# Kernel tuning notes

Measured on AMD Instinct MI355X. Metric: run time of the kernel, lower is better.

The kernel has to match this reference:

```python
import jax, jax.numpy as jnp
import numpy as np

N_HEAD = 8

def setup_inputs() -> dict:
    key = jax.random.key(0)
    ks = jax.random.split(key, 5)
    N, C, T, V = 64, 128, 64, 25
    x = jax.random.normal(ks[0], (N, C, T, V), dtype=jnp.float32)
    Wa = jax.random.normal(ks[1], (C, C), dtype=jnp.float32) * (1.0 / np.sqrt(C))
    ba = jax.random.normal(ks[2], (C,), dtype=jnp.float32) * 0.01
    Wp = jax.random.normal(ks[3], (C, C), dtype=jnp.float32) * (1.0 / np.sqrt(C))
    bp = jax.random.normal(ks[4], (C,), dtype=jnp.float32) * 0.01
    temp = jnp.ones((N_HEAD, 1), dtype=jnp.float32)
    denom_bias = jnp.zeros((N_HEAD, 1, 1), dtype=jnp.float32)
    return {"x": x, "Wa": Wa, "ba": ba, "Wp": Wp, "bp": bp, "temp": temp, "denom_bias": denom_bias}

def reference(x, Wa, ba, Wp, bp, temp, denom_bias):
    # x: (N, C, T, V); eval mode (dropout = identity); residual = identity (in==out, stride==1)
    N, C, T, V = x.shape
    H = N_HEAD
    hd = C // H
    res = x
    # 1x1 conv c_attn
    w = jnp.einsum('nctv,oc->notv', x, Wa) + ba[None, :, None, None]
    # (N,H,hd,T,V) -> (N,H,T,V,hd) -> (N,H,T*V,hd)
    w = w.reshape(N, H, hd, T, V).transpose(0, 1, 3, 4, 2).reshape(N, H, T * V, hd)
    w_sq = w * w
    denom = jnp.maximum(jnp.cumsum(w_sq, axis=2), 1e-12)
    w_normed = w_sq / denom + denom_bias  # denom_bias (H,1,1) broadcasts
    tmp = jnp.sum(w_normed, axis=-1) * temp  # (N,H,L) * (H,1)
    Pi = jax.nn.softmax(tmp, axis=2)  # (N,H,L)
    dots = jnp.cumsum(w_sq * Pi[..., None], axis=2) / (jnp.cumsum(Pi, axis=2) + 1e-8)[..., None]
    attn = 1.0 / (1.0 + dots)
    y = -(w * Pi[..., None]) * attn  # (N,H,L,hd)
    y = y.reshape(N, H, T, V, hd).transpose(0, 1, 4, 2, 3).reshape(N, C, T, V)
    y = jnp.einsum('nctv,oc->notv', y, Wp) + bp[None, :, None, None]
    y = y + res
    return jax.nn.relu(y)
```

## Files before the change

kernel.cpp:

```cpp
#include <hip/hip_runtime.h>
#include <hip/hip_bf16.h>

#define N_S     64
#define C_CH    128
#define L_SEQ   1600
#define H_HEADS 8
#define HD      16
#define SEGN    64
#define SEGL    25
#define PADW    136
#define PADT    70
#define NHD     13312
#define NHU     26624

typedef __attribute__((ext_vector_type(8))) short bf16x8;
typedef __attribute__((ext_vector_type(4))) float f32x4;

__device__ inline unsigned short f2bf(float f) {
  return __builtin_bit_cast(unsigned short, __float2bfloat16(f));
}
__device__ inline float bflo(unsigned int u) { return __builtin_bit_cast(float, u << 16); }
__device__ inline float bfhi(unsigned int u) { return __builtin_bit_cast(float, u & 0xffff0000u); }
__device__ inline unsigned int pk(float a, float b) {
  return (unsigned int)f2bf(a) | ((unsigned int)f2bf(b) << 16);
}

template <int CTRL>
__device__ inline float dppadd(float x) {
  int r = __builtin_amdgcn_update_dpp(0, __builtin_bit_cast(int, x), CTRL, 0xF, 0xF, true);
  return x + __builtin_bit_cast(float, r);
}


__global__ __launch_bounds__(256) void k_gemm1(const float* __restrict__ x,
                                               const float* __restrict__ Wa,
                                               const float* __restrict__ ba,
                                               unsigned short* __restrict__ w3u) {
  __shared__ unsigned short was[128 * PADW];
  __shared__ unsigned short xs[128 * PADT];
  const int n = blockIdx.y;
  const int l0 = blockIdx.x * 64;
  const int t = threadIdx.x;
  const float* xn = x + (size_t)n * (C_CH * L_SEQ);

#pragma unroll
  for (int it = 0; it < 16; ++it) {
    int pos = it * 256 + t;
    int o = pos >> 5;
    int c4 = (pos & 31) << 2;
    float4 v = *reinterpret_cast<const float4*>(Wa + o * C_CH + c4);
    ushort4 u;
    u.x = f2bf(v.x); u.y = f2bf(v.y); u.z = f2bf(v.z); u.w = f2bf(v.w);
    *reinterpret_cast<ushort4*>(&was[o * PADW + c4]) = u;
  }
#pragma unroll
  for (int it = 0; it < 8; ++it) {
    int pos = it * 256 + t;
    int c = pos >> 4;
    int l4 = (pos & 15) << 2;
    float4 v = *reinterpret_cast<const float4*>(xn + (size_t)c * L_SEQ + l0 + l4);
    ushort4 u;
    u.x = f2bf(v.x); u.y = f2bf(v.y); u.z = f2bf(v.z); u.w = f2bf(v.w);
    *reinterpret_cast<ushort4*>(&xs[c * PADT + l4]) = u;
  }
  __syncthreads();

  const int wv = t >> 6;
  const int lane = t & 63;
  const int r16 = lane & 15;
  const int kg = lane >> 4;
  f32x4 acc[8];
#pragma unroll
  for (int ot = 0; ot < 8; ++ot) acc[ot] = (f32x4){0.f, 0.f, 0.f, 0.f};

#pragma unroll
  for (int ks = 0; ks < 4; ++ks) {
    bf16x8 a;
#pragma unroll
    for (int j = 0; j < 8; ++j)
      a[j] = (short)xs[(ks * 32 + kg * 8 + j) * PADT + wv * 16 + r16];
#pragma unroll
    for (int ot = 0; ot < 8; ++ot) {
      bf16x8 b = *reinterpret_cast<const bf16x8*>(&was[(ot * 16 + r16) * PADW + ks * 32 + kg * 8]);
      acc[ot] = __builtin_amdgcn_mfma_f32_16x16x32_bf16(a, b, acc[ot], 0, 0, 0);
    }
  }
  const int lbase = l0 + wv * 16 + kg * 4;
  unsigned int idxA[4];
#pragma unroll
  for (int i = 0; i < 4; ++i) {
    unsigned int l = (unsigned int)(lbase + i);
    unsigned int sg = l / 25u;
    unsigned int j = l - sg * 25u;
    idxA[i] = (j >> 1) * 2048u + sg * 32u + ((unsigned int)r16 << 1) + (j & 1u);
  }
  unsigned short* w3n = w3u + (size_t)(n * H_HEADS) * NHU;
#pragma unroll
  for (int ot = 0; ot < 8; ++ot) {
    float bav = ba[ot * 16 + r16];
    unsigned short* p = w3n + (size_t)ot * NHU;
#pragma unroll
    for (int i = 0; i < 4; ++i)
      p[idxA[i]] = f2bf(acc[ot][i] + bav);
  }
}

__global__ __launch_bounds__(1024) void k_scan(const unsigned int* __restrict__ w3d,
                                               unsigned int* __restrict__ y3d,
                                               const float* __restrict__ temp,
                                               const float* __restrict__ dbias) {
  __shared__ float stot[SEGN][17];
  __shared__ float red[16];

  const int nh = blockIdx.x;
  const int h = nh & 7;
  const int t = threadIdx.x;
  const int d = t & 15;
  const int lane = t & 63;
  const int wv = t >> 6;
  const int seg = t >> 4;
  const float tscale = temp[h];
  const float db16 = 16.f * dbias[h];
  const float M = fmaxf((16.f + db16) * tscale, db16 * tscale);
  const float A = tscale * 1.44269504088896f;
  const float B = (db16 * tscale - M) * 1.44269504088896f;

  unsigned int vp[13];
  const unsigned int* srcd = w3d + (size_t)nh * NHD;
#pragma unroll
  for (int ii = 0; ii < 13; ++ii) vp[ii] = srcd[ii * 1024 + t];

  float tot = 0.f;
#pragma unroll
  for (int i = 0; i < SEGL; ++i) {
    float v = (i & 1) ? bfhi(vp[i >> 1]) : bflo(vp[i >> 1]);
    tot += v * v;
  }
  stot[seg][d] = tot;
  __syncthreads();
  {
    float val = stot[lane][wv];
#pragma unroll
    for (int sh = 1; sh < 64; sh <<= 1) {
      float nv = __shfl_up(val, sh);
      if (lane >= sh) val += nv;
    }
    stot[lane][wv] = val;
  }
  __syncthreads();
  const float off = stot[seg][d] - tot;

  unsigned int ep[13];
  float run = off;
  float sAcc = 0.f, wpAcc = 0.f;
  float eprev = 0.f;
#pragma unroll
  for (int i = 0; i < SEGL; ++i) {
    float v = (i & 1) ? bfhi(vp[i >> 1]) : bflo(vp[i >> 1]);
    float wsq = v * v;
    run += wsq;
    float c = __fdividef(wsq, fmaxf(run, 1e-12f));
    c = dppadd<0x128>(c);
    c = dppadd<0x124>(c);
    c = dppadd<0x122>(c);
    c = dppadd<0x121>(c);
    float e = exp2f(fmaf(c, A, B));
    sAcc += e;
    wpAcc = fmaf(wsq, e, wpAcc);
    if (i & 1) ep[i >> 1] = pk(eprev, e); else eprev = e;
  }
  ep[12] = pk(eprev, 0.f);
  {
    float s = sAcc;
#pragma unroll
    for (int mask = 32; mask; mask >>= 1) s += __shfl_xor(s, mask);
    if (lane == 0) red[wv] = s;
  }
  __syncthreads();
  float S16 = 0.f;
#pragma unroll
  for (int i2 = 0; i2 < 16; ++i2) S16 += red[i2];
  const float S = S16 * 0.0625f;
  const float ninvS = -1.0f / S;
  const float epsS = 1e-8f * S;

  stot[seg][d] = wpAcc;
  if (d == 0) stot[seg][16] = sAcc;
  __syncthreads();
  {
    float val = stot[lane][wv];
#pragma unroll
    for (int sh = 1; sh < 64; sh <<= 1) {
      float nv = __shfl_up(val, sh);
      if (lane >= sh) val += nv;
    }
    stot[lane][wv] = val;
    if (wv == 0) {
      float val2 = stot[lane][16];
#pragma unroll
      for (int sh = 1; sh < 64; sh <<= 1) {
        float nv = __shfl_up(val2, sh);
        if (lane >= sh) val2 += nv;
      }
      stot[lane][16] = val2;
    }
  }
  __syncthreads();
  const float wp_off = stot[seg][d] - wpAcc;
  const float pi_off = stot[seg][16] - sAcc;

  {
    float run_wp = wp_off, run_pi = pi_off;
    float ylo = 0.f;
#pragma unroll
    for (int i = 0; i < SEGL; ++i) {
      float v = (i & 1) ? bfhi(vp[i >> 1]) : bflo(vp[i >> 1]);
      float e = (i & 1) ? bfhi(ep[i >> 1]) : bflo(ep[i >> 1]);
      run_pi += e;
      run_wp = fmaf(v * v, e, run_wp);
      float dn = run_pi + epsS;
      float y = (v * e) * __fdividef(dn, dn + run_wp) * ninvS;
      if (i & 1) vp[i >> 1] = pk(ylo, y); else ylo = y;
    }
    vp[12] = pk(ylo, 0.f);
  }
  unsigned int* dstd = y3d + (size_t)nh * NHD;
#pragma unroll
  for (int ii = 0; ii < 13; ++ii) dstd[ii * 1024 + t] = vp[ii];
}

__global__ __launch_bounds__(256) void k_gemm2(const unsigned short* __restrict__ y3u,
                                               const float* __restrict__ Wp,
                                               const float* __restrict__ bp,
                                               const float* __restrict__ x,
                                               float* __restrict__ out) {
  __shared__ unsigned short wps[128 * PADW];
  __shared__ unsigned short ys[128 * PADT];
  const int n = blockIdx.y;
  const int l0 = blockIdx.x * 64;
  const int t = threadIdx.x;

#pragma unroll
  for (int it = 0; it < 16; ++it) {
    int pos = it * 256 + t;
    int o = pos >> 5;
    int c4 = (pos & 31) << 2;
    float4 v = *reinterpret_cast<const float4*>(Wp + o * C_CH + c4);
    ushort4 u;
    u.x = f2bf(v.x); u.y = f2bf(v.y); u.z = f2bf(v.z); u.w = f2bf(v.w);
    *reinterpret_cast<ushort4*>(&wps[o * PADW + c4]) = u;
  }
#pragma unroll
  for (int k = 0; k < 32; ++k) {
    int e = k * 256 + t;
    int lloc = e >> 7;
    int c = e & 127;
    unsigned int l = (unsigned int)(l0 + lloc);
    unsigned int sg = l / 25u;
    unsigned int j = l - sg * 25u;
    unsigned short v = y3u[(size_t)(n * H_HEADS + (c >> 4)) * NHU +
                           (j >> 1) * 2048u + sg * 32u + ((unsigned int)(c & 15) << 1) + (j & 1u)];
    ys[c * PADT + lloc] = v;
  }
  __syncthreads();

  const int wv = t >> 6;
  const int lane = t & 63;
  const int r16 = lane & 15;
  const int kg = lane >> 4;
  f32x4 acc[8];
#pragma unroll
  for (int ot = 0; ot < 8; ++ot) acc[ot] = (f32x4){0.f, 0.f, 0.f, 0.f};

#pragma unroll
  for (int ks = 0; ks < 4; ++ks) {
    bf16x8 b;
#pragma unroll
    for (int j = 0; j < 8; ++j)
      b[j] = (short)ys[(ks * 32 + kg * 8 + j) * PADT + wv * 16 + r16];
#pragma unroll
    for (int ot = 0; ot < 8; ++ot) {
      bf16x8 a = *reinterpret_cast<const bf16x8*>(&wps[(ot * 16 + r16) * PADW + ks * 32 + kg * 8]);
      acc[ot] = __builtin_amdgcn_mfma_f32_16x16x32_bf16(a, b, acc[ot], 0, 0, 0);
    }
  }
  const int gl = l0 + wv * 16 + r16;
#pragma unroll
  for (int ot = 0; ot < 8; ++ot) {
#pragma unroll
    for (int i = 0; i < 4; ++i) {
      int o = ot * 16 + kg * 4 + i;
      size_t idx = (size_t)n * (C_CH * L_SEQ) + (size_t)o * L_SEQ + gl;
      float r = acc[ot][i] + bp[o] + x[idx];
      out[idx] = fmaxf(r, 0.f);
    }
  }
}

extern "C" void kernel_launch(void* const* d_in, const int* in_sizes, int n_in,
                              void* d_out, int out_size, void* d_ws, size_t ws_size,
                              hipStream_t stream) {
  const float* x     = (const float*)d_in[0];
  const float* Wa    = (const float*)d_in[1];
  const float* ba    = (const float*)d_in[2];
  const float* Wp    = (const float*)d_in[3];
  const float* bp    = (const float*)d_in[4];
  const float* temp  = (const float*)d_in[5];
  const float* dbias = (const float*)d_in[6];
  float* out = (float*)d_out;

  unsigned short* w3u = (unsigned short*)d_ws;
  unsigned short* y3u = w3u + (size_t)N_S * H_HEADS * NHU;

  k_gemm1<<<dim3(L_SEQ / 64, N_S), 256, 0, stream>>>(x, Wa, ba, w3u);
  k_scan<<<N_S * H_HEADS, 1024, 0, stream>>>((const unsigned int*)w3u, (unsigned int*)y3u, temp, dbias);
  k_gemm2<<<dim3(L_SEQ / 64, N_S), 256, 0, stream>>>(y3u, Wp, bp, x, out);
}
```

Baseline: 83.65 us.

## Fuse first projection GEMM into per-head scan kernel via shared-memory slab

Merges the c_attn GEMM into the scan kernel: each (sample, head) block computes its 16 output channels over the full sequence in 256-column chunks and stores them in a shared-memory slab laid out for the scan. This removes the intermediate global write/read of the projected activations and one launch. The scan result is written in plain channel-major layout so the second GEMM can load it with vectorized 16-byte loads. In exchange, every head block re-reads and re-converts the whole input sample, roughly 8x redundant x traffic. The large shared footprint and serial chunk loop may also limit occupancy.

```diff
diff --git a/kernel.cpp b/kernel.cpp
--- a/kernel.cpp
+++ b/kernel.cpp
@@ -9,9 +9,9 @@
 #define SEGN    64
 #define SEGL    25
 #define PADW    136
-#define PADT    70
-#define NHD     13312
-#define NHU     26624
+#define PADX    270
+#define PADY    72
+#define SROW    839
 
 typedef __attribute__((ext_vector_type(8))) short bf16x8;
 typedef __attribute__((ext_vector_type(4))) float f32x4;
@@ -31,93 +31,77 @@
   return x + __builtin_bit_cast(float, r);
 }
 
-
-__global__ __launch_bounds__(256) void k_gemm1(const float* __restrict__ x,
-                                               const float* __restrict__ Wa,
-                                               const float* __restrict__ ba,
-                                               unsigned short* __restrict__ w3u) {
-  __shared__ unsigned short was[128 * PADW];
-  __shared__ unsigned short xs[128 * PADT];
-  const int n = blockIdx.y;
-  const int l0 = blockIdx.x * 64;
+__global__ __launch_bounds__(1024) void k_fused(const float* __restrict__ x,
+                                                const float* __restrict__ Wa,
+                                                const float* __restrict__ ba,
+                                                const float* __restrict__ temp,
+                                                const float* __restrict__ dbias,
+                                                unsigned short* __restrict__ y2) {
+  __shared__ unsigned short was[16 * PADW];
+  __shared__ unsigned short xs[128 * PADX];
+  __shared__ unsigned int slabd[16 * SROW];
+  __shared__ float stot[SEGN][17];
+  __shared__ float red[16];
+  unsigned short* slab = (unsigned short*)slabd;
+
+  const int bid = blockIdx.x;
+  const int nh = (bid & 7) * 64 + (bid >> 3);
+  const int n = nh >> 3;
+  const int h = nh & 7;
   const int t = threadIdx.x;
-  const float* xn = x + (size_t)n * (C_CH * L_SEQ);
-
-#pragma unroll
-  for (int it = 0; it < 16; ++it) {
-    int pos = it * 256 + t;
-    int o = pos >> 5;
-    int c4 = (pos & 31) << 2;
-    float4 v = *reinterpret_cast<const float4*>(Wa + o * C_CH + c4);
-    ushort4 u;
-    u.x = f2bf(v.x); u.y = f2bf(v.y); u.z = f2bf(v.z); u.w = f2bf(v.w);
-    *reinterpret_cast<ushort4*>(&was[o * PADW + c4]) = u;
-  }
-#pragma unroll
-  for (int it = 0; it < 8; ++it) {
-    int pos = it * 256 + t;
-    int c = pos >> 4;
-    int l4 = (pos & 15) << 2;
-    float4 v = *reinterpret_cast<const float4*>(xn + (size_t)c * L_SEQ + l0 + l4);
-    ushort4 u;
-    u.x = f2bf(v.x); u.y = f2bf(v.y); u.z = f2bf(v.z); u.w = f2bf(v.w);
-    *reinterpret_cast<ushort4*>(&xs[c * PADT + l4]) = u;
-  }
-  __syncthreads();
-
+  const int lane = t & 63;
   const int wv = t >> 6;
-  const int lane = t & 63;
   const int r16 = lane & 15;
   const int kg = lane >> 4;
-  f32x4 acc[8];
-#pragma unroll
-  for (int ot = 0; ot < 8; ++ot) acc[ot] = (f32x4){0.f, 0.f, 0.f, 0.f};
-
-#pragma unroll
-  for (int ks = 0; ks < 4; ++ks) {
-    bf16x8 a;
-#pragma unroll
-    for (int j = 0; j < 8; ++j)
-      a[j] = (short)xs[(ks * 32 + kg * 8 + j) * PADT + wv * 16 + r16];
-#pragma unroll
-    for (int ot = 0; ot < 8; ++ot) {
-      bf16x8 b = *reinterpret_cast<const bf16x8*>(&was[(ot * 16 + r16) * PADW + ks * 32 + kg * 8]);
-      acc[ot] = __builtin_amdgcn_mfma_f32_16x16x32_bf16(a, b, acc[ot], 0, 0, 0);
-    }
-  }
-  const int lbase = l0 + wv * 16 + kg * 4;
-  unsigned int idxA[4];
-#pragma unroll
-  for (int i = 0; i < 4; ++i) {
-    unsigned int l = (unsigned int)(lbase + i);
-    unsigned int sg = l / 25u;
-    unsigned int j = l - sg * 25u;
-    idxA[i] = (j >> 1) * 2048u + sg * 32u + ((unsigned int)r16 << 1) + (j & 1u);
-  }
-  unsigned short* w3n = w3u + (size_t)(n * H_HEADS) * NHU;
-#pragma unroll
-  for (int ot = 0; ot < 8; ++ot) {
-    float bav = ba[ot * 16 + r16];
-    unsigned short* p = w3n + (size_t)ot * NHU;
-#pragma unroll
-    for (int i = 0; i < 4; ++i)
-      p[idxA[i]] = f2bf(acc[ot][i] + bav);
-  }
-}
-
-__global__ __launch_bounds__(1024) void k_scan(const unsigned int* __restrict__ w3d,
-                                               unsigned int* __restrict__ y3d,
-                                               const float* __restrict__ temp,
-                                               const float* __restrict__ dbias) {
-  __shared__ float stot[SEGN][17];
-  __shared__ float red[16];
-
-  const int nh = blockIdx.x;
-  const int h = nh & 7;
-  const int t = threadIdx.x;
-  const int d = t & 15;
-  const int lane = t & 63;
-  const int wv = t >> 6;
+  const float* xn = x + (size_t)n * (C_CH * L_SEQ);
+
+#pragma unroll
+  for (int it = 0; it < 2; ++it) {
+    int pos = it * 1024 + t;
+    int orow = pos >> 7, c = pos & 127;
+    was[orow * PADW + c] = f2bf(Wa[(h * 16 + orow) * C_CH + c]);
+  }
+  const float bav = ba[h * 16 + r16];
+
+  for (int ck = 0; ck < 7; ++ck) {
+    const int l0 = ck * 256;
+    const int CL = (ck < 6) ? 256 : 64;
+    __syncthreads();
+    const int nE = (C_CH * CL) >> 2;
+    for (int pos = t; pos < nE; pos += 1024) {
+      int c, l4;
+      if (CL == 256) { c = pos >> 6; l4 = (pos & 63) << 2; }
+      else           { c = pos >> 4; l4 = (pos & 15) << 2; }
+      float4 v = *reinterpret_cast<const float4*>(xn + (size_t)c * L_SEQ + l0 + l4);
+      ushort4 u;
+      u.x = f2bf(v.x); u.y = f2bf(v.y); u.z = f2bf(v.z); u.w = f2bf(v.w);
+      *reinterpret_cast<ushort4*>(&xs[c * PADX + l4]) = u;
+    }
+    __syncthreads();
+    if (wv * 16 < CL) {
+      f32x4 acc = (f32x4){0.f, 0.f, 0.f, 0.f};
+#pragma unroll
+      for (int ks = 0; ks < 4; ++ks) {
+        bf16x8 a;
+#pragma unroll
+        for (int j = 0; j < 8; ++j)
+          a[j] = (short)xs[(ks * 32 + kg * 8 + j) * PADX + wv * 16 + r16];
+        bf16x8 b = *reinterpret_cast<const bf16x8*>(&was[r16 * PADW + ks * 32 + kg * 8]);
+        acc = __builtin_amdgcn_mfma_f32_16x16x32_bf16(a, b, acc, 0, 0, 0);
+      }
+      const int lbase = l0 + wv * 16 + kg * 4;
+#pragma unroll
+      for (int i = 0; i < 4; ++i) {
+        int l = lbase + i;
+        int sg = l / 25;
+        int j = l - sg * 25;
+        slab[r16 * (2 * SROW) + sg * 26 + j] = f2bf(acc[i] + bav);
+      }
+    }
+  }
+  __syncthreads();
+
+  const int d = r16;
   const int seg = t >> 4;
   const float tscale = temp[h];
   const float db16 = 16.f * dbias[h];
@@ -126,9 +110,9 @@
   const float B = (db16 * tscale - M) * 1.44269504088896f;
 
   unsigned int vp[13];
-  const unsigned int* srcd = w3d + (size_t)nh * NHD;
-#pragma unroll
-  for (int ii = 0; ii < 13; ++ii) vp[ii] = srcd[ii * 1024 + t];
+  const int rbq = d * SROW + seg * 13;
+#pragma unroll
+  for (int ii = 0; ii < 13; ++ii) vp[ii] = slabd[rbq + ii];
 
   float tot = 0.f;
 #pragma unroll
@@ -224,18 +208,34 @@
     }
     vp[12] = pk(ylo, 0.f);
   }
-  unsigned int* dstd = y3d + (size_t)nh * NHD;
-#pragma unroll
-  for (int ii = 0; ii < 13; ++ii) dstd[ii * 1024 + t] = vp[ii];
-}
-
-__global__ __launch_bounds__(256) void k_gemm2(const unsigned short* __restrict__ y3u,
+#pragma unroll
+  for (int ii = 0; ii < 13; ++ii) slabd[rbq + ii] = vp[ii];
+  __syncthreads();
+  unsigned int* y2dw = reinterpret_cast<unsigned int*>(y2) + (size_t)nh * 12800;
+#pragma unroll
+  for (int k = 0; k < 13; ++k) {
+    int g = k * 1024 + t;
+    if (g < 12800) {
+      int row = g / 800;
+      int gl = g - row * 800;
+      int l = gl * 2;
+      int sg = l / 25;
+      int j = l - sg * 25;
+      int base = row * (2 * SROW) + sg * 26 + j;
+      unsigned int lo = slab[base];
+      unsigned int hi = slab[base + 1 + (j == 24 ? 1 : 0)];
+      y2dw[g] = lo | (hi << 16);
+    }
+  }
+}
+
+__global__ __launch_bounds__(256) void k_gemm2(const unsigned short* __restrict__ y2,
                                                const float* __restrict__ Wp,
                                                const float* __restrict__ bp,
                                                const float* __restrict__ x,
                                                float* __restrict__ out) {
   __shared__ unsigned short wps[128 * PADW];
-  __shared__ unsigned short ys[128 * PADT];
+  __shared__ unsigned short ys[128 * PADY];
   const int n = blockIdx.y;
   const int l0 = blockIdx.x * 64;
   const int t = threadIdx.x;
@@ -251,16 +251,12 @@
     *reinterpret_cast<ushort4*>(&wps[o * PADW + c4]) = u;
   }
 #pragma unroll
-  for (int k = 0; k < 32; ++k) {
-    int e = k * 256 + t;
-    int lloc = e >> 7;
-    int c = e & 127;
-    unsigned int l = (unsigned int)(l0 + lloc);
-    unsigned int sg = l / 25u;
-    unsigned int j = l - sg * 25u;
-    unsigned short v = y3u[(size_t)(n * H_HEADS + (c >> 4)) * NHU +
-                           (j >> 1) * 2048u + sg * 32u + ((unsigned int)(c & 15) << 1) + (j & 1u)];
-    ys[c * PADT + lloc] = v;
+  for (int it = 0; it < 4; ++it) {
+    int pos = it * 256 + t;
+    int c = pos >> 3;
+    int l8 = (pos & 7) << 3;
+    uint4 v = *reinterpret_cast<const uint4*>(y2 + ((size_t)n * C_CH + c) * L_SEQ + l0 + l8);
+    *reinterpret_cast<uint4*>(&ys[c * PADY + l8]) = v;
   }
   __syncthreads();
 
@@ -277,7 +273,7 @@
     bf16x8 b;
 #pragma unroll
     for (int j = 0; j < 8; ++j)
-      b[j] = (short)ys[(ks * 32 + kg * 8 + j) * PADT + wv * 16 + r16];
+      b[j] = (short)ys[(ks * 32 + kg * 8 + j) * PADY + wv * 16 + r16];
 #pragma unroll
     for (int ot = 0; ot < 8; ++ot) {
       bf16x8 a = *reinterpret_cast<const bf16x8*>(&wps[(ot * 16 + r16) * PADW + ks * 32 + kg * 8]);
@@ -309,10 +305,8 @@
   const float* dbias = (const float*)d_in[6];
   float* out = (float*)d_out;
 
-  unsigned short* w3u = (unsigned short*)d_ws;
-  unsigned short* y3u = w3u + (size_t)N_S * H_HEADS * NHU;
-
-  k_gemm1<<<dim3(L_SEQ / 64, N_S), 256, 0, stream>>>(x, Wa, ba, w3u);
-  k_scan<<<N_S * H_HEADS, 1024, 0, stream>>>((const unsigned int*)w3u, (unsigned int*)y3u, temp, dbias);
-  k_gemm2<<<dim3(L_SEQ / 64, N_S), 256, 0, stream>>>(y3u, Wp, bp, x, out);
-}
+  unsigned short* y2 = (unsigned short*)d_ws;
+
+  k_fused<<<N_S * H_HEADS, 1024, 0, stream>>>(x, Wa, ba, temp, dbias, y2);
+  k_gemm2<<<dim3(L_SEQ / 64, N_S), 256, 0, stream>>>(y2, Wp, bp, x, out);
+}
```

New measurement: 101.6 us. +21.5%, slower.
